# Kernel tuning notes

Hardware: AMD Instinct MI355X
Metric: run time of the kernel (lower is better)

Reference implementation:

```python
import jax, jax.numpy as jnp
import numpy as np

# Repo globals / config
VOCAB_SIZE = 14
TOK_DIM = 8
POS_DIM = 8
D_MODEL = TOK_DIM + POS_DIM  # 16
MAX_SEQ_LEN = 2048
N_HEADS = 2
HEAD_DIM = 3
ATTN_DIM = N_HEADS * HEAD_DIM  # 6
FFN_DIM = 3
B, T = 16, 2048
EPS = 1e-5


def _ln(x, w, b):
    m = jnp.mean(x, axis=-1, keepdims=True)
    v = jnp.var(x, axis=-1, keepdims=True)
    return (x - m) * jax.lax.rsqrt(v + EPS) * w + b


def setup_inputs() -> dict:
    key = jax.random.key(0)
    ks = jax.random.split(key, 20)
    g = lambda k, shape: (jax.random.normal(k, shape, jnp.float32) * 0.1)
    return {
        "idx": jax.random.randint(ks[0], (B, T), 0, VOCAB_SIZE),
        "tok_emb": g(ks[1], (VOCAB_SIZE, TOK_DIM)),
        "pos_enc": g(ks[2], (MAX_SEQ_LEN, POS_DIM)),
        "Wq": g(ks[3], (ATTN_DIM, POS_DIM)),
        "Wk": g(ks[4], (ATTN_DIM, POS_DIM)),
        "Wv": g(ks[5], (ATTN_DIM, TOK_DIM)),
        "Wo": g(ks[6], (D_MODEL, ATTN_DIM)),
        "ln1_w": jnp.ones((D_MODEL,), jnp.float32),
        "ln1_b": jnp.zeros((D_MODEL,), jnp.float32),
        "ln2_w": jnp.ones((D_MODEL,), jnp.float32),
        "ln2_b": jnp.zeros((D_MODEL,), jnp.float32),
        "lnf_w": jnp.ones((D_MODEL,), jnp.float32),
        "lnf_b": jnp.zeros((D_MODEL,), jnp.float32),
        "W1": g(ks[7], (FFN_DIM, D_MODEL)),
        "b1": jnp.zeros((FFN_DIM,), jnp.float32),
        "W2": g(ks[8], (D_MODEL, FFN_DIM)),
        "b2": jnp.zeros((D_MODEL,), jnp.float32),
        "Wh": g(ks[9], (TOK_DIM, D_MODEL)),
    }


def reference(idx, tok_emb, pos_enc, Wq, Wk, Wv, Wo,
              ln1_w, ln1_b, ln2_w, ln2_b, lnf_w, lnf_b,
              W1, b1, W2, b2, Wh):
    Bq, Tq = idx.shape
    tok = tok_emb[idx]                                  # [B,T,TOK_DIM]
    pos = jnp.broadcast_to(pos_enc[:Tq][None], (Bq, Tq, POS_DIM))
    x = jnp.concatenate([tok, pos], axis=-1)            # [B,T,D_MODEL]
    h = _ln(x, ln1_w, ln1_b)
    x_tok = h[..., :TOK_DIM]
    x_pos = h[..., TOK_DIM:]
    # projections (torch Linear: y = x @ W.T)
    q = (x_pos @ Wq.T).reshape(Bq, Tq, N_HEADS, HEAD_DIM).transpose(0, 2, 1, 3)
    k = (x_pos @ Wk.T).reshape(Bq, Tq, N_HEADS, HEAD_DIM).transpose(0, 2, 1, 3)
    v = (x_tok @ Wv.T).reshape(Bq, Tq, N_HEADS, HEAD_DIM).transpose(0, 2, 1, 3)
    scores = jnp.einsum('bhqd,bhkd->bhqk', q, k) / jnp.sqrt(jnp.float32(HEAD_DIM))
    mask = jnp.tril(jnp.ones((Tq, Tq), dtype=bool))
    scores = jnp.where(mask[None, None], scores, -jnp.inf)
    attn = jax.nn.softmax(scores, axis=-1)
    out = jnp.einsum('bhqk,bhkd->bhqd', attn, v)
    out = out.transpose(0, 2, 1, 3).reshape(Bq, Tq, ATTN_DIM)
    x = x + out @ Wo.T
    h2 = _ln(x, ln2_w, ln2_b)
    x = x + (jax.nn.gelu(h2 @ W1.T + b1, approximate=False) @ W2.T + b2)
    x = _ln(x, lnf_w, lnf_b)
    return (x @ Wh.T) @ tok_emb.T                       # tied head -> [B,T,VOCAB]
```

## Files before the change

### kernel.cpp

```cpp
#include <hip/hip_runtime.h>
#include <hip/hip_fp16.h>
#include <math.h>

#define BB    16
#define TT    2048
#define VOCAB 14
#define TOKD  8
#define POSD  8
#define DM    16
#define NH    2
#define HD    3
#define AD    6
#define FFND  3

#define NTOK  (BB*TT)
#define BH    (BB*NH)
#define TPB   36
#define NTILE (BH*TPB)

struct P {
    const int*   idx;
    const float* tok_emb;
    const float* pos_enc;
    const float* Wq;
    const float* Wk;
    const float* Wv;
    const float* Wo;
    const float* ln1w;
    const float* ln1b;
    const float* ln2w;
    const float* ln2b;
    const float* lnfw;
    const float* lnfb;
    const float* W1;
    const float* b1;
    const float* W2;
    const float* b2;
    const float* Wh;
    float*       out;
    float4*      pbuf;
};

__device__ __forceinline__ void ln1_h(const P& p, int b, int t, float* h) {
    float x[DM];
    int tok = p.idx[b * TT + t];
    #pragma unroll
    for (int j = 0; j < TOKD; ++j) x[j]        = p.tok_emb[tok * TOKD + j];
    #pragma unroll
    for (int j = 0; j < POSD; ++j) x[TOKD + j] = p.pos_enc[t * POSD + j];
    float m = 0.f;
    #pragma unroll
    for (int j = 0; j < DM; ++j) m += x[j];
    m *= (1.f / DM);
    float v = 0.f;
    #pragma unroll
    for (int j = 0; j < DM; ++j) { float d = x[j] - m; v += d * d; }
    v *= (1.f / DM);
    float rs = rsqrtf(v + 1e-5f);
    #pragma unroll
    for (int j = 0; j < DM; ++j)
        h[j] = (x[j] - m) * rs * p.ln1w[j] + p.ln1b[j];
}

__global__ __launch_bounds__(256) void attn_kernel(P p) {
    __shared__ uint4  skv[256];
    __shared__ float4 sq[256];
    __shared__ float4 spart[1024];

    const int tid  = threadIdx.x;
    int tile = blockIdx.x;
    int bh   = tile / TPB;
    int r    = tile - bh * TPB;
    int s    = 0;
    while (((s + 1) * (s + 2)) / 2 <= r) ++s;
    int c    = r - (s * (s + 1)) / 2;
    int b    = bh >> 1, head = bh & 1;

    const float QS = 1.4426950408889634f / 1.7320508075688772f;

    {
        int t = (c << 8) + tid;
        float h[DM];
        ln1_h(p, b, t, h);
        float k[HD], v[HD];
        #pragma unroll
        for (int d = 0; d < HD; ++d) {
            int a = head * HD + d;
            float sk = 0.f, sv = 0.f;
            #pragma unroll
            for (int j = 0; j < 8; ++j) {
                sk = fmaf(p.Wk[a * 8 + j], h[TOKD + j], sk);
                sv = fmaf(p.Wv[a * 8 + j], h[j], sv);
            }
            k[d] = sk; v[d] = sv;
        }
        __half2 h0 = __floats2half2_rn(k[0], k[1]);
        __half2 h1 = __floats2half2_rn(k[2], v[0]);
        __half2 h2 = __floats2half2_rn(v[1], v[2]);
        uint4 rec;
        rec.x = *reinterpret_cast<unsigned int*>(&h0);
        rec.y = *reinterpret_cast<unsigned int*>(&h1);
        rec.z = *reinterpret_cast<unsigned int*>(&h2);
        rec.w = 0u;
        skv[tid] = rec;
        if (c == s) {
            float q[HD];
            #pragma unroll
            for (int d = 0; d < HD; ++d) {
                int a = head * HD + d;
                float sqv = 0.f;
                #pragma unroll
                for (int j = 0; j < 8; ++j)
                    sqv = fmaf(p.Wq[a * 8 + j], h[TOKD + j], sqv);
                q[d] = sqv;
            }
            sq[tid] = make_float4(q[0] * QS, q[1] * QS, q[2] * QS, 0.f);
        }
    }
    if (c != s) {
        int t = (s << 8) + tid;
        float h[DM];
        ln1_h(p, b, t, h);
        float q[HD];
        #pragma unroll
        for (int d = 0; d < HD; ++d) {
            int a = head * HD + d;
            float sqv = 0.f;
            #pragma unroll
            for (int j = 0; j < 8; ++j)
                sqv = fmaf(p.Wq[a * 8 + j], h[TOKD + j], sqv);
            q[d] = sqv;
        }
        sq[tid] = make_float4(q[0] * QS, q[1] * QS, q[2] * QS, 0.f);
    }
    __syncthreads();

    int wv   = tid >> 6;
    int lane = tid & 63;
    int kw   = wv << 6;
    float4 q0 = sq[lane];
    float4 q1 = sq[64 + lane];
    float4 q2 = sq[128 + lane];
    float4 q3 = sq[192 + lane];

    float l0=0.f,a00=0.f,a10=0.f,a20=0.f;
    float l1=0.f,a01=0.f,a11=0.f,a21=0.f;
    float l2=0.f,a02=0.f,a12=0.f,a22=0.f;
    float l3=0.f,a03=0.f,a13=0.f,a23=0.f;

    if (c < s) {
        #pragma unroll 4
        for (int it = 0; it < 64; ++it) {
            uint4 rec = skv[kw + it];
            float2 f0 = __half22float2(*reinterpret_cast<const __half2*>(&rec.x));
            float2 f1 = __half22float2(*reinterpret_cast<const __half2*>(&rec.y));
            float2 f2 = __half22float2(*reinterpret_cast<const __half2*>(&rec.z));
            float k0 = f0.x, k1 = f0.y, k2 = f1.x;
            float v0 = f1.y, v1 = f2.x, v2 = f2.y;
            float pr;
            pr = exp2f(fmaf(q0.x,k0,fmaf(q0.y,k1,q0.z*k2)));
            l0+=pr; a00=fmaf(pr,v0,a00); a10=fmaf(pr,v1,a10); a20=fmaf(pr,v2,a20);
            pr = exp2f(fmaf(q1.x,k0,fmaf(q1.y,k1,q1.z*k2)));
            l1+=pr; a01=fmaf(pr,v0,a01); a11=fmaf(pr,v1,a11); a21=fmaf(pr,v2,a21);
            pr = exp2f(fmaf(q2.x,k0,fmaf(q2.y,k1,q2.z*k2)));
            l2+=pr; a02=fmaf(pr,v0,a02); a12=fmaf(pr,v1,a12); a22=fmaf(pr,v2,a22);
            pr = exp2f(fmaf(q3.x,k0,fmaf(q3.y,k1,q3.z*k2)));
            l3+=pr; a03=fmaf(pr,v0,a03); a13=fmaf(pr,v1,a13); a23=fmaf(pr,v2,a23);
        }
    } else {
        #pragma unroll 4
        for (int it = 0; it < 64; ++it) {
            int kr = kw + it;
            uint4 rec = skv[kw + it];
            float2 f0 = __half22float2(*reinterpret_cast<const __half2*>(&rec.x));
            float2 f1 = __half22float2(*reinterpret_cast<const __half2*>(&rec.y));
            float2 f2 = __half22float2(*reinterpret_cast<const __half2*>(&rec.z));
            float k0 = f0.x, k1 = f0.y, k2 = f1.x;
            float v0 = f1.y, v1 = f2.x, v2 = f2.y;
            float pr;
            pr = exp2f(fmaf(q0.x,k0,fmaf(q0.y,k1,q0.z*k2)));
            pr = (kr <= lane)       ? pr : 0.f;
            l0+=pr; a00=fmaf(pr,v0,a00); a10=fmaf(pr,v1,a10); a20=fmaf(pr,v2,a20);
            pr = exp2f(fmaf(q1.x,k0,fmaf(q1.y,k1,q1.z*k2)));
            pr = (kr <= 64 + lane)  ? pr : 0.f;
            l1+=pr; a01=fmaf(pr,v0,a01); a11=fmaf(pr,v1,a11); a21=fmaf(pr,v2,a21);
            pr = exp2f(fmaf(q2.x,k0,fmaf(q2.y,k1,q2.z*k2)));
            pr = (kr <= 128 + lane) ? pr : 0.f;
            l2+=pr; a02=fmaf(pr,v0,a02); a12=fmaf(pr,v1,a12); a22=fmaf(pr,v2,a22);
            pr = exp2f(fmaf(q3.x,k0,fmaf(q3.y,k1,q3.z*k2)));
            pr = (kr <= 192 + lane) ? pr : 0.f;
            l3+=pr; a03=fmaf(pr,v0,a03); a13=fmaf(pr,v1,a13); a23=fmaf(pr,v2,a23);
        }
    }

    spart[(wv << 8) + lane]       = make_float4(a00, a10, a20, l0);
    spart[(wv << 8) + 64 + lane]  = make_float4(a01, a11, a21, l1);
    spart[(wv << 8) + 128 + lane] = make_float4(a02, a12, a22, l2);
    spart[(wv << 8) + 192 + lane] = make_float4(a03, a13, a23, l3);
    __syncthreads();

    float4 p0 = spart[tid];
    float4 p1 = spart[256 + tid];
    float4 p2 = spart[512 + tid];
    float4 p3 = spart[768 + tid];
    float4 acc = make_float4(p0.x+p1.x+p2.x+p3.x, p0.y+p1.y+p2.y+p3.y,
                             p0.z+p1.z+p2.z+p3.z, p0.w+p1.w+p2.w+p3.w);
    p.pbuf[((size_t)bh * 8 + c) * TT + (s << 8) + tid] = acc;
}

__global__ __launch_bounds__(256) void epi_kernel(P p) {
    int gid = blockIdx.x * 256 + threadIdx.x;
    if (gid >= NTOK) return;
    int t = gid & (TT - 1);
    int b = gid >> 11;
    int s = t >> 8;

    float x[DM];
    int tok = p.idx[gid];
    #pragma unroll
    for (int j = 0; j < TOKD; ++j) x[j]        = p.tok_emb[tok * TOKD + j];
    #pragma unroll
    for (int j = 0; j < POSD; ++j) x[TOKD + j] = p.pos_enc[t * POSD + j];

    float att[AD];
    #pragma unroll
    for (int hh = 0; hh < NH; ++hh) {
        const float4* pp = p.pbuf + ((size_t)(b * NH + hh) * 8) * TT + t;
        float4 acc = pp[0];
        for (int c = 1; c <= s; ++c) {
            float4 e = pp[(size_t)c * TT];
            acc.x += e.x; acc.y += e.y; acc.z += e.z; acc.w += e.w;
        }
        float inv = 1.f / acc.w;
        att[hh*3+0] = acc.x * inv;
        att[hh*3+1] = acc.y * inv;
        att[hh*3+2] = acc.z * inv;
    }

    float xo[DM];
    #pragma unroll
    for (int j = 0; j < DM; ++j) {
        float sacc = x[j];
        #pragma unroll
        for (int a = 0; a < AD; ++a) sacc = fmaf(p.Wo[j * AD + a], att[a], sacc);
        xo[j] = sacc;
    }

    float m = 0.f;
    #pragma unroll
    for (int j = 0; j < DM; ++j) m += xo[j];
    m *= (1.f / DM);
    float v = 0.f;
    #pragma unroll
    for (int j = 0; j < DM; ++j) { float d = xo[j] - m; v += d * d; }
    v *= (1.f / DM);
    float rs = rsqrtf(v + 1e-5f);
    float h2[DM];
    #pragma unroll
    for (int j = 0; j < DM; ++j)
        h2[j] = (xo[j] - m) * rs * p.ln2w[j] + p.ln2b[j];

    float g[FFND];
    #pragma unroll
    for (int cc = 0; cc < FFND; ++cc) {
        float f = p.b1[cc];
        #pragma unroll
        for (int j = 0; j < DM; ++j) f = fmaf(p.W1[cc * DM + j], h2[j], f);
        g[cc] = 0.5f * f * (1.f + erff(f * 0.70710678118654752f));
    }
    float x2[DM];
    #pragma unroll
    for (int j = 0; j < DM; ++j) {
        float sacc = xo[j] + p.b2[j];
        #pragma unroll
        for (int cc = 0; cc < FFND; ++cc) sacc = fmaf(p.W2[j * FFND + cc], g[cc], sacc);
        x2[j] = sacc;
    }

    m = 0.f;
    #pragma unroll
    for (int j = 0; j < DM; ++j) m += x2[j];
    m *= (1.f / DM);
    v = 0.f;
    #pragma unroll
    for (int j = 0; j < DM; ++j) { float d = x2[j] - m; v += d * d; }
    v *= (1.f / DM);
    rs = rsqrtf(v + 1e-5f);
    float y[DM];
    #pragma unroll
    for (int j = 0; j < DM; ++j)
        y[j] = (x2[j] - m) * rs * p.lnfw[j] + p.lnfb[j];

    float t8[TOKD];
    #pragma unroll
    for (int pp = 0; pp < TOKD; ++pp) {
        float sacc = 0.f;
        #pragma unroll
        for (int j = 0; j < DM; ++j) sacc = fmaf(p.Wh[pp * DM + j], y[j], sacc);
        t8[pp] = sacc;
    }
    float* op = p.out + (size_t)gid * VOCAB;
    #pragma unroll
    for (int vcb = 0; vcb < VOCAB; ++vcb) {
        float sacc = 0.f;
        #pragma unroll
        for (int pp = 0; pp < TOKD; ++pp)
            sacc = fmaf(t8[pp], p.tok_emb[vcb * TOKD + pp], sacc);
        op[vcb] = sacc;
    }
}

extern "C" void kernel_launch(void* const* d_in, const int* in_sizes, int n_in,
                              void* d_out, int out_size, void* d_ws, size_t ws_size,
                              hipStream_t stream) {
    P p;
    p.idx     = (const int*)d_in[0];
    p.tok_emb = (const float*)d_in[1];
    p.pos_enc = (const float*)d_in[2];
    p.Wq      = (const float*)d_in[3];
    p.Wk      = (const float*)d_in[4];
    p.Wv      = (const float*)d_in[5];
    p.Wo      = (const float*)d_in[6];
    p.ln1w    = (const float*)d_in[7];
    p.ln1b    = (const float*)d_in[8];
    p.ln2w    = (const float*)d_in[9];
    p.ln2b    = (const float*)d_in[10];
    p.lnfw    = (const float*)d_in[11];
    p.lnfb    = (const float*)d_in[12];
    p.W1      = (const float*)d_in[13];
    p.b1      = (const float*)d_in[14];
    p.W2      = (const float*)d_in[15];
    p.b2      = (const float*)d_in[16];
    p.Wh      = (const float*)d_in[17];
    p.out     = (float*)d_out;
    p.pbuf    = (float4*)d_ws;

    attn_kernel<<<NTILE, 256, 0, stream>>>(p);
    epi_kernel<<<NTOK / 256, 256, 0, stream>>>(p);
}
```

Baseline: 135.8 us.

## Fuse epilogue into attention kernel via last-block atomic counter

```diff
diff --git a/kernel.cpp b/kernel.cpp
--- a/kernel.cpp
+++ b/kernel.cpp
@@ -39,6 +39,7 @@
     const float* Wh;
     float*       out;
     float4*      pbuf;
+    int*         cnt;
 };
 
 __device__ __forceinline__ void ln1_h(const P& p, int b, int t, float* h) {
@@ -60,12 +61,112 @@
     #pragma unroll
     for (int j = 0; j < DM; ++j)
         h[j] = (x[j] - m) * rs * p.ln1w[j] + p.ln1b[j];
+}
+
+__device__ __forceinline__ void do_epi_token(const P& p, int b, int t) {
+    int s   = t >> 8;
+    int gid = b * TT + t;
+
+    float x[DM];
+    int tok = p.idx[gid];
+    #pragma unroll
+    for (int j = 0; j < TOKD; ++j) x[j]        = p.tok_emb[tok * TOKD + j];
+    #pragma unroll
+    for (int j = 0; j < POSD; ++j) x[TOKD + j] = p.pos_enc[t * POSD + j];
+
+    float att[AD];
+    #pragma unroll
+    for (int hh = 0; hh < NH; ++hh) {
+        const float4* pp = p.pbuf + ((size_t)(b * NH + hh) * 8) * TT + t;
+        float4 acc = pp[0];
+        for (int c = 1; c <= s; ++c) {
+            float4 e = pp[(size_t)c * TT];
+            acc.x += e.x; acc.y += e.y; acc.z += e.z; acc.w += e.w;
+        }
+        float inv = 1.f / acc.w;
+        att[hh*3+0] = acc.x * inv;
+        att[hh*3+1] = acc.y * inv;
+        att[hh*3+2] = acc.z * inv;
+    }
+
+    float xo[DM];
+    #pragma unroll
+    for (int j = 0; j < DM; ++j) {
+        float sacc = x[j];
+        #pragma unroll
+        for (int a = 0; a < AD; ++a) sacc = fmaf(p.Wo[j * AD + a], att[a], sacc);
+        xo[j] = sacc;
+    }
+
+    float m = 0.f;
+    #pragma unroll
+    for (int j = 0; j < DM; ++j) m += xo[j];
+    m *= (1.f / DM);
+    float v = 0.f;
+    #pragma unroll
+    for (int j = 0; j < DM; ++j) { float d = xo[j] - m; v += d * d; }
+    v *= (1.f / DM);
+    float rs = rsqrtf(v + 1e-5f);
+    float h2[DM];
+    #pragma unroll
+    for (int j = 0; j < DM; ++j)
+        h2[j] = (xo[j] - m) * rs * p.ln2w[j] + p.ln2b[j];
+
+    float g[FFND];
+    #pragma unroll
+    for (int cc = 0; cc < FFND; ++cc) {
+        float f = p.b1[cc];
+        #pragma unroll
+        for (int j = 0; j < DM; ++j) f = fmaf(p.W1[cc * DM + j], h2[j], f);
+        g[cc] = 0.5f * f * (1.f + erff(f * 0.70710678118654752f));
+    }
+    float x2[DM];
+    #pragma unroll
+    for (int j = 0; j < DM; ++j) {
+        float sacc = xo[j] + p.b2[j];
+        #pragma unroll
+        for (int cc = 0; cc < FFND; ++cc) sacc = fmaf(p.W2[j * FFND + cc], g[cc], sacc);
+        x2[j] = sacc;
+    }
+
+    m = 0.f;
+    #pragma unroll
+    for (int j = 0; j < DM; ++j) m += x2[j];
+    m *= (1.f / DM);
+    v = 0.f;
+    #pragma unroll
+    for (int j = 0; j < DM; ++j) { float d = x2[j] - m; v += d * d; }
+    v *= (1.f / DM);
+    rs = rsqrtf(v + 1e-5f);
+    float y[DM];
+    #pragma unroll
+    for (int j = 0; j < DM; ++j)
+        y[j] = (x2[j] - m) * rs * p.lnfw[j] + p.lnfb[j];
+
+    float t8[TOKD];
+    #pragma unroll
+    for (int pp = 0; pp < TOKD; ++pp) {
+        float sacc = 0.f;
+        #pragma unroll
+        for (int j = 0; j < DM; ++j) sacc = fmaf(p.Wh[pp * DM + j], y[j], sacc);
+        t8[pp] = sacc;
+    }
+    float* op = p.out + (size_t)gid * VOCAB;
+    #pragma unroll
+    for (int vcb = 0; vcb < VOCAB; ++vcb) {
+        float sacc = 0.f;
+        #pragma unroll
+        for (int pp = 0; pp < TOKD; ++pp)
+            sacc = fmaf(t8[pp], p.tok_emb[vcb * TOKD + pp], sacc);
+        op[vcb] = sacc;
+    }
 }
 
 __global__ __launch_bounds__(256) void attn_kernel(P p) {
     __shared__ uint4  skv[256];
     __shared__ float4 sq[256];
     __shared__ float4 spart[1024];
+    __shared__ int    lastFlag;
 
     const int tid  = threadIdx.x;
     int tile = blockIdx.x;
@@ -158,13 +259,13 @@
             float k0 = f0.x, k1 = f0.y, k2 = f1.x;
             float v0 = f1.y, v1 = f2.x, v2 = f2.y;
             float pr;
-            pr = exp2f(fmaf(q0.x,k0,fmaf(q0.y,k1,q0.z*k2)));
+            pr = __builtin_amdgcn_exp2f(fmaf(q0.x,k0,fmaf(q0.y,k1,q0.z*k2)));
             l0+=pr; a00=fmaf(pr,v0,a00); a10=fmaf(pr,v1,a10); a20=fmaf(pr,v2,a20);
-            pr = exp2f(fmaf(q1.x,k0,fmaf(q1.y,k1,q1.z*k2)));
+            pr = __builtin_amdgcn_exp2f(fmaf(q1.x,k0,fmaf(q1.y,k1,q1.z*k2)));
             l1+=pr; a01=fmaf(pr,v0,a01); a11=fmaf(pr,v1,a11); a21=fmaf(pr,v2,a21);
-            pr = exp2f(fmaf(q2.x,k0,fmaf(q2.y,k1,q2.z*k2)));
+            pr = __builtin_amdgcn_exp2f(fmaf(q2.x,k0,fmaf(q2.y,k1,q2.z*k2)));
             l2+=pr; a02=fmaf(pr,v0,a02); a12=fmaf(pr,v1,a12); a22=fmaf(pr,v2,a22);
-            pr = exp2f(fmaf(q3.x,k0,fmaf(q3.y,k1,q3.z*k2)));
+            pr = __builtin_amdgcn_exp2f(fmaf(q3.x,k0,fmaf(q3.y,k1,q3.z*k2)));
             l3+=pr; a03=fmaf(pr,v0,a03); a13=fmaf(pr,v1,a13); a23=fmaf(pr,v2,a23);
         }
     } else {
@@ -178,16 +279,16 @@
             float k0 = f0.x, k1 = f0.y, k2 = f1.x;
             float v0 = f1.y, v1 = f2.x, v2 = f2.y;
             float pr;
-            pr = exp2f(fmaf(q0.x,k0,fmaf(q0.y,k1,q0.z*k2)));
+            pr = __builtin_amdgcn_exp2f(fmaf(q0.x,k0,fmaf(q0.y,k1,q0.z*k2)));
             pr = (kr <= lane)       ? pr : 0.f;
             l0+=pr; a00=fmaf(pr,v0,a00); a10=fmaf(pr,v1,a10); a20=fmaf(pr,v2,a20);
-            pr = exp2f(fmaf(q1.x,k0,fmaf(q1.y,k1,q1.z*k2)));
+            pr = __builtin_amdgcn_exp2f(fmaf(q1.x,k0,fmaf(q1.y,k1,q1.z*k2)));
             pr = (kr <= 64 + lane)  ? pr : 0.f;
             l1+=pr; a01=fmaf(pr,v0,a01); a11=fmaf(pr,v1,a11); a21=fmaf(pr,v2,a21);
-            pr = exp2f(fmaf(q2.x,k0,fmaf(q2.y,k1,q2.z*k2)));
+            pr = __builtin_amdgcn_exp2f(fmaf(q2.x,k0,fmaf(q2.y,k1,q2.z*k2)));
             pr = (kr <= 128 + lane) ? pr : 0.f;
             l2+=pr; a02=fmaf(pr,v0,a02); a12=fmaf(pr,v1,a12); a22=fmaf(pr,v2,a22);
-            pr = exp2f(fmaf(q3.x,k0,fmaf(q3.y,k1,q3.z*k2)));
+            pr = __builtin_amdgcn_exp2f(fmaf(q3.x,k0,fmaf(q3.y,k1,q3.z*k2)));
             pr = (kr <= 192 + lane) ? pr : 0.f;
             l3+=pr; a03=fmaf(pr,v0,a03); a13=fmaf(pr,v1,a13); a23=fmaf(pr,v2,a23);
         }
@@ -206,107 +307,17 @@
     float4 acc = make_float4(p0.x+p1.x+p2.x+p3.x, p0.y+p1.y+p2.y+p3.y,
                              p0.z+p1.z+p2.z+p3.z, p0.w+p1.w+p2.w+p3.w);
     p.pbuf[((size_t)bh * 8 + c) * TT + (s << 8) + tid] = acc;
-}
-
-__global__ __launch_bounds__(256) void epi_kernel(P p) {
-    int gid = blockIdx.x * 256 + threadIdx.x;
-    if (gid >= NTOK) return;
-    int t = gid & (TT - 1);
-    int b = gid >> 11;
-    int s = t >> 8;
-
-    float x[DM];
-    int tok = p.idx[gid];
-    #pragma unroll
-    for (int j = 0; j < TOKD; ++j) x[j]        = p.tok_emb[tok * TOKD + j];
-    #pragma unroll
-    for (int j = 0; j < POSD; ++j) x[TOKD + j] = p.pos_enc[t * POSD + j];
-
-    float att[AD];
-    #pragma unroll
-    for (int hh = 0; hh < NH; ++hh) {
-        const float4* pp = p.pbuf + ((size_t)(b * NH + hh) * 8) * TT + t;
-        float4 acc = pp[0];
-        for (int c = 1; c <= s; ++c) {
-            float4 e = pp[(size_t)c * TT];
-            acc.x += e.x; acc.y += e.y; acc.z += e.z; acc.w += e.w;
-        }
-        float inv = 1.f / acc.w;
-        att[hh*3+0] = acc.x * inv;
-        att[hh*3+1] = acc.y * inv;
-        att[hh*3+2] = acc.z * inv;
-    }
-
-    float xo[DM];
-    #pragma unroll
-    for (int j = 0; j < DM; ++j) {
-        float sacc = x[j];
-        #pragma unroll
-        for (int a = 0; a < AD; ++a) sacc = fmaf(p.Wo[j * AD + a], att[a], sacc);
-        xo[j] = sacc;
-    }
-
-    float m = 0.f;
-    #pragma unroll
-    for (int j = 0; j < DM; ++j) m += xo[j];
-    m *= (1.f / DM);
-    float v = 0.f;
-    #pragma unroll
-    for (int j = 0; j < DM; ++j) { float d = xo[j] - m; v += d * d; }
-    v *= (1.f / DM);
-    float rs = rsqrtf(v + 1e-5f);
-    float h2[DM];
-    #pragma unroll
-    for (int j = 0; j < DM; ++j)
-        h2[j] = (xo[j] - m) * rs * p.ln2w[j] + p.ln2b[j];
-
-    float g[FFND];
-    #pragma unroll
-    for (int cc = 0; cc < FFND; ++cc) {
-        float f = p.b1[cc];
-        #pragma unroll
-        for (int j = 0; j < DM; ++j) f = fmaf(p.W1[cc * DM + j], h2[j], f);
-        g[cc] = 0.5f * f * (1.f + erff(f * 0.70710678118654752f));
-    }
-    float x2[DM];
-    #pragma unroll
-    for (int j = 0; j < DM; ++j) {
-        float sacc = xo[j] + p.b2[j];
-        #pragma unroll
-        for (int cc = 0; cc < FFND; ++cc) sacc = fmaf(p.W2[j * FFND + cc], g[cc], sacc);
-        x2[j] = sacc;
-    }
-
-    m = 0.f;
-    #pragma unroll
-    for (int j = 0; j < DM; ++j) m += x2[j];
-    m *= (1.f / DM);
-    v = 0.f;
-    #pragma unroll
-    for (int j = 0; j < DM; ++j) { float d = x2[j] - m; v += d * d; }
-    v *= (1.f / DM);
-    rs = rsqrtf(v + 1e-5f);
-    float y[DM];
-    #pragma unroll
-    for (int j = 0; j < DM; ++j)
-        y[j] = (x2[j] - m) * rs * p.lnfw[j] + p.lnfb[j];
-
-    float t8[TOKD];
-    #pragma unroll
-    for (int pp = 0; pp < TOKD; ++pp) {
-        float sacc = 0.f;
-        #pragma unroll
-        for (int j = 0; j < DM; ++j) sacc = fmaf(p.Wh[pp * DM + j], y[j], sacc);
-        t8[pp] = sacc;
-    }
-    float* op = p.out + (size_t)gid * VOCAB;
-    #pragma unroll
-    for (int vcb = 0; vcb < VOCAB; ++vcb) {
-        float sacc = 0.f;
-        #pragma unroll
-        for (int pp = 0; pp < TOKD; ++pp)
-            sacc = fmaf(t8[pp], p.tok_emb[vcb * TOKD + pp], sacc);
-        op[vcb] = sacc;
+
+    __threadfence();
+    __syncthreads();
+    if (tid == 0) {
+        int old = atomicAdd(&p.cnt[b * 8 + s], 1);
+        lastFlag = (old == 2 * (s + 1) - 1) ? 1 : 0;
+    }
+    __syncthreads();
+    if (lastFlag) {
+        __threadfence();
+        do_epi_token(p, b, (s << 8) + tid);
     }
 }
 
@@ -334,7 +345,8 @@
     p.Wh      = (const float*)d_in[17];
     p.out     = (float*)d_out;
     p.pbuf    = (float4*)d_ws;
-
+    p.cnt     = (int*)((char*)d_ws + (size_t)8 * 1024 * 1024);
+
+    hipMemsetAsync(p.cnt, 0, BB * 8 * sizeof(int), stream);
     attn_kernel<<<NTILE, 256, 0, stream>>>(p);
-    epi_kernel<<<NTOK / 256, 256, 0, stream>>>(p);
 }
```

After: 245.8 us. 1.81x slower.

## Precompute LN1 and QKV in a prep kernel; skip masked diagonal sub-blocks

Applied to the files above, without the earlier changes.

```diff
diff --git a/kernel.cpp b/kernel.cpp
--- a/kernel.cpp
+++ b/kernel.cpp
@@ -38,16 +38,24 @@
     const float* b2;
     const float* Wh;
     float*       out;
+    float4*      qbuf;
+    uint4*       kvh;
     float4*      pbuf;
 };
 
-__device__ __forceinline__ void ln1_h(const P& p, int b, int t, float* h) {
+__global__ __launch_bounds__(256) void prep_kernel(P p) {
+    int gid = blockIdx.x * 256 + threadIdx.x;
+    if (gid >= NTOK) return;
+    int t = gid & (TT - 1);
+    int b = gid >> 11;
+
     float x[DM];
-    int tok = p.idx[b * TT + t];
+    int tok = p.idx[gid];
     #pragma unroll
     for (int j = 0; j < TOKD; ++j) x[j]        = p.tok_emb[tok * TOKD + j];
     #pragma unroll
     for (int j = 0; j < POSD; ++j) x[TOKD + j] = p.pos_enc[t * POSD + j];
+
     float m = 0.f;
     #pragma unroll
     for (int j = 0; j < DM; ++j) m += x[j];
@@ -57,10 +65,47 @@
     for (int j = 0; j < DM; ++j) { float d = x[j] - m; v += d * d; }
     v *= (1.f / DM);
     float rs = rsqrtf(v + 1e-5f);
+    float h[DM];
     #pragma unroll
     for (int j = 0; j < DM; ++j)
         h[j] = (x[j] - m) * rs * p.ln1w[j] + p.ln1b[j];
+
+    float q[AD], k[AD], vv[AD];
+    #pragma unroll
+    for (int a = 0; a < AD; ++a) {
+        float sq = 0.f, sk = 0.f, sv = 0.f;
+        #pragma unroll
+        for (int j = 0; j < 8; ++j) {
+            sq = fmaf(p.Wq[a * 8 + j], h[TOKD + j], sq);
+            sk = fmaf(p.Wk[a * 8 + j], h[TOKD + j], sk);
+            sv = fmaf(p.Wv[a * 8 + j], h[j], sv);
+        }
+        q[a] = sq; k[a] = sk; vv[a] = sv;
+    }
+
+    const float QS = 1.4426950408889634f / 1.7320508075688772f;
+    #pragma unroll
+    for (int hh = 0; hh < NH; ++hh) {
+        size_t base = (size_t)(b * NH + hh) * TT + t;
+        p.qbuf[base] = make_float4(q[hh*3] * QS, q[hh*3+1] * QS, q[hh*3+2] * QS, 0.f);
+        __half2 h0 = __floats2half2_rn(k[hh*3],    k[hh*3+1]);
+        __half2 h1 = __floats2half2_rn(k[hh*3+2],  vv[hh*3]);
+        __half2 h2 = __floats2half2_rn(vv[hh*3+1], vv[hh*3+2]);
+        uint4 rec;
+        rec.x = *reinterpret_cast<unsigned int*>(&h0);
+        rec.y = *reinterpret_cast<unsigned int*>(&h1);
+        rec.z = *reinterpret_cast<unsigned int*>(&h2);
+        rec.w = 0u;
+        p.kvh[base] = rec;
+    }
 }
+
+#define UNPACK_REC(rec)                                                        \
+    float2 f0 = __half22float2(*reinterpret_cast<const __half2*>(&rec.x));     \
+    float2 f1 = __half22float2(*reinterpret_cast<const __half2*>(&rec.y));     \
+    float2 f2 = __half22float2(*reinterpret_cast<const __half2*>(&rec.z));     \
+    float k0 = f0.x, k1 = f0.y, k2 = f1.x;                                     \
+    float v0 = f1.y, v1 = f2.x, v2 = f2.y;
 
 __global__ __launch_bounds__(256) void attn_kernel(P p) {
     __shared__ uint4  skv[256];
@@ -74,129 +119,76 @@
     int s    = 0;
     while (((s + 1) * (s + 2)) / 2 <= r) ++s;
     int c    = r - (s * (s + 1)) / 2;
-    int b    = bh >> 1, head = bh & 1;
-
-    const float QS = 1.4426950408889634f / 1.7320508075688772f;
-
-    {
-        int t = (c << 8) + tid;
-        float h[DM];
-        ln1_h(p, b, t, h);
-        float k[HD], v[HD];
-        #pragma unroll
-        for (int d = 0; d < HD; ++d) {
-            int a = head * HD + d;
-            float sk = 0.f, sv = 0.f;
-            #pragma unroll
-            for (int j = 0; j < 8; ++j) {
-                sk = fmaf(p.Wk[a * 8 + j], h[TOKD + j], sk);
-                sv = fmaf(p.Wv[a * 8 + j], h[j], sv);
-            }
-            k[d] = sk; v[d] = sv;
-        }
-        __half2 h0 = __floats2half2_rn(k[0], k[1]);
-        __half2 h1 = __floats2half2_rn(k[2], v[0]);
-        __half2 h2 = __floats2half2_rn(v[1], v[2]);
-        uint4 rec;
-        rec.x = *reinterpret_cast<unsigned int*>(&h0);
-        rec.y = *reinterpret_cast<unsigned int*>(&h1);
-        rec.z = *reinterpret_cast<unsigned int*>(&h2);
-        rec.w = 0u;
-        skv[tid] = rec;
-        if (c == s) {
-            float q[HD];
-            #pragma unroll
-            for (int d = 0; d < HD; ++d) {
-                int a = head * HD + d;
-                float sqv = 0.f;
-                #pragma unroll
-                for (int j = 0; j < 8; ++j)
-                    sqv = fmaf(p.Wq[a * 8 + j], h[TOKD + j], sqv);
-                q[d] = sqv;
-            }
-            sq[tid] = make_float4(q[0] * QS, q[1] * QS, q[2] * QS, 0.f);
-        }
-    }
-    if (c != s) {
-        int t = (s << 8) + tid;
-        float h[DM];
-        ln1_h(p, b, t, h);
-        float q[HD];
-        #pragma unroll
-        for (int d = 0; d < HD; ++d) {
-            int a = head * HD + d;
-            float sqv = 0.f;
-            #pragma unroll
-            for (int j = 0; j < 8; ++j)
-                sqv = fmaf(p.Wq[a * 8 + j], h[TOKD + j], sqv);
-            q[d] = sqv;
-        }
-        sq[tid] = make_float4(q[0] * QS, q[1] * QS, q[2] * QS, 0.f);
-    }
+
+    skv[tid] = p.kvh [(size_t)bh * TT + (c << 8) + tid];
+    sq [tid] = p.qbuf[(size_t)bh * TT + (s << 8) + tid];
     __syncthreads();
 
     int wv   = tid >> 6;
     int lane = tid & 63;
     int kw   = wv << 6;
-    float4 q0 = sq[lane];
-    float4 q1 = sq[64 + lane];
-    float4 q2 = sq[128 + lane];
-    float4 q3 = sq[192 + lane];
-
-    float l0=0.f,a00=0.f,a10=0.f,a20=0.f;
-    float l1=0.f,a01=0.f,a11=0.f,a21=0.f;
-    float l2=0.f,a02=0.f,a12=0.f,a22=0.f;
-    float l3=0.f,a03=0.f,a13=0.f,a23=0.f;
+
+    float4 qr[4];
+    #pragma unroll
+    for (int j = 0; j < 4; ++j) qr[j] = sq[(j << 6) + lane];
+
+    float ac[4][4];
+    #pragma unroll
+    for (int j = 0; j < 4; ++j)
+        ac[j][0] = ac[j][1] = ac[j][2] = ac[j][3] = 0.f;
 
     if (c < s) {
         #pragma unroll 4
         for (int it = 0; it < 64; ++it) {
             uint4 rec = skv[kw + it];
-            float2 f0 = __half22float2(*reinterpret_cast<const __half2*>(&rec.x));
-            float2 f1 = __half22float2(*reinterpret_cast<const __half2*>(&rec.y));
-            float2 f2 = __half22float2(*reinterpret_cast<const __half2*>(&rec.z));
-            float k0 = f0.x, k1 = f0.y, k2 = f1.x;
-            float v0 = f1.y, v1 = f2.x, v2 = f2.y;
-            float pr;
-            pr = exp2f(fmaf(q0.x,k0,fmaf(q0.y,k1,q0.z*k2)));
-            l0+=pr; a00=fmaf(pr,v0,a00); a10=fmaf(pr,v1,a10); a20=fmaf(pr,v2,a20);
-            pr = exp2f(fmaf(q1.x,k0,fmaf(q1.y,k1,q1.z*k2)));
-            l1+=pr; a01=fmaf(pr,v0,a01); a11=fmaf(pr,v1,a11); a21=fmaf(pr,v2,a21);
-            pr = exp2f(fmaf(q2.x,k0,fmaf(q2.y,k1,q2.z*k2)));
-            l2+=pr; a02=fmaf(pr,v0,a02); a12=fmaf(pr,v1,a12); a22=fmaf(pr,v2,a22);
-            pr = exp2f(fmaf(q3.x,k0,fmaf(q3.y,k1,q3.z*k2)));
-            l3+=pr; a03=fmaf(pr,v0,a03); a13=fmaf(pr,v1,a13); a23=fmaf(pr,v2,a23);
+            UNPACK_REC(rec)
+            #pragma unroll
+            for (int j = 0; j < 4; ++j) {
+                float sc = fmaf(qr[j].x, k0, fmaf(qr[j].y, k1, qr[j].z * k2));
+                float pr = __builtin_amdgcn_exp2f(sc);
+                ac[j][0] = fmaf(pr, v0, ac[j][0]);
+                ac[j][1] = fmaf(pr, v1, ac[j][1]);
+                ac[j][2] = fmaf(pr, v2, ac[j][2]);
+                ac[j][3] += pr;
+            }
         }
     } else {
-        #pragma unroll 4
-        for (int it = 0; it < 64; ++it) {
-            int kr = kw + it;
-            uint4 rec = skv[kw + it];
-            float2 f0 = __half22float2(*reinterpret_cast<const __half2*>(&rec.x));
-            float2 f1 = __half22float2(*reinterpret_cast<const __half2*>(&rec.y));
-            float2 f2 = __half22float2(*reinterpret_cast<const __half2*>(&rec.z));
-            float k0 = f0.x, k1 = f0.y, k2 = f1.x;
-            float v0 = f1.y, v1 = f2.x, v2 = f2.y;
-            float pr;
-            pr = exp2f(fmaf(q0.x,k0,fmaf(q0.y,k1,q0.z*k2)));
-            pr = (kr <= lane)       ? pr : 0.f;
-            l0+=pr; a00=fmaf(pr,v0,a00); a10=fmaf(pr,v1,a10); a20=fmaf(pr,v2,a20);
-            pr = exp2f(fmaf(q1.x,k0,fmaf(q1.y,k1,q1.z*k2)));
-            pr = (kr <= 64 + lane)  ? pr : 0.f;
-            l1+=pr; a01=fmaf(pr,v0,a01); a11=fmaf(pr,v1,a11); a21=fmaf(pr,v2,a21);
-            pr = exp2f(fmaf(q2.x,k0,fmaf(q2.y,k1,q2.z*k2)));
-            pr = (kr <= 128 + lane) ? pr : 0.f;
-            l2+=pr; a02=fmaf(pr,v0,a02); a12=fmaf(pr,v1,a12); a22=fmaf(pr,v2,a22);
-            pr = exp2f(fmaf(q3.x,k0,fmaf(q3.y,k1,q3.z*k2)));
-            pr = (kr <= 192 + lane) ? pr : 0.f;
-            l3+=pr; a03=fmaf(pr,v0,a03); a13=fmaf(pr,v1,a13); a23=fmaf(pr,v2,a23);
+        #pragma unroll
+        for (int j = 0; j < 4; ++j) {
+            if (j < wv) continue;
+            if (j == wv) {
+                #pragma unroll 4
+                for (int it = 0; it < 64; ++it) {
+                    uint4 rec = skv[kw + it];
+                    UNPACK_REC(rec)
+                    float sc = fmaf(qr[j].x, k0, fmaf(qr[j].y, k1, qr[j].z * k2));
+                    float pr = __builtin_amdgcn_exp2f(sc);
+                    pr = (it <= lane) ? pr : 0.f;
+                    ac[j][0] = fmaf(pr, v0, ac[j][0]);
+                    ac[j][1] = fmaf(pr, v1, ac[j][1]);
+                    ac[j][2] = fmaf(pr, v2, ac[j][2]);
+                    ac[j][3] += pr;
+                }
+            } else {
+                #pragma unroll 4
+                for (int it = 0; it < 64; ++it) {
+                    uint4 rec = skv[kw + it];
+                    UNPACK_REC(rec)
+                    float sc = fmaf(qr[j].x, k0, fmaf(qr[j].y, k1, qr[j].z * k2));
+                    float pr = __builtin_amdgcn_exp2f(sc);
+                    ac[j][0] = fmaf(pr, v0, ac[j][0]);
+                    ac[j][1] = fmaf(pr, v1, ac[j][1]);
+                    ac[j][2] = fmaf(pr, v2, ac[j][2]);
+                    ac[j][3] += pr;
+                }
+            }
         }
     }
 
-    spart[(wv << 8) + lane]       = make_float4(a00, a10, a20, l0);
-    spart[(wv << 8) + 64 + lane]  = make_float4(a01, a11, a21, l1);
-    spart[(wv << 8) + 128 + lane] = make_float4(a02, a12, a22, l2);
-    spart[(wv << 8) + 192 + lane] = make_float4(a03, a13, a23, l3);
+    #pragma unroll
+    for (int j = 0; j < 4; ++j)
+        spart[(wv << 8) + (j << 6) + lane] =
+            make_float4(ac[j][0], ac[j][1], ac[j][2], ac[j][3]);
     __syncthreads();
 
     float4 p0 = spart[tid];
@@ -333,8 +325,11 @@
     p.b2      = (const float*)d_in[16];
     p.Wh      = (const float*)d_in[17];
     p.out     = (float*)d_out;
-    p.pbuf    = (float4*)d_ws;
-
+    p.qbuf    = (float4*)d_ws;
+    p.kvh     = (uint4*)((char*)d_ws + (1u << 20));
+    p.pbuf    = (float4*)((char*)d_ws + (2u << 20));
+
+    prep_kernel<<<NTOK / 256, 256, 0, stream>>>(p);
     attn_kernel<<<NTILE, 256, 0, stream>>>(p);
     epi_kernel<<<NTOK / 256, 256, 0, stream>>>(p);
 }
```

After: 131.1 us. 3.5% less time.
